# Performance work log

Measured on AMD Instinct MI355X. Metric: run time of the kernel, lower is better.

## Reference

```python
import jax, jax.numpy as jnp
import numpy as np

B, T = 64, 2048
HID, FAST, SLOW, VOCAB = 256, 64, 256, 64
WRITE_THRESH = 0.4
NEG = -1000000000.0


def setup_inputs() -> dict:
    key = jax.random.key(0)
    ks = jax.random.split(key, 10)
    s = 0.05  # small init so gate sigmoids are not saturated
    return {
        "seq": jax.random.randint(ks[0], (B, T), 0, VOCAB),
        "emb": jax.random.normal(ks[1], (VOCAB, HID), jnp.float32),        # encoder embedding table
        "Wg": jax.random.normal(ks[2], (HID, 1), jnp.float32) * s,         # write_gate
        "bg": jnp.zeros((1,), jnp.float32),
        "Wd": jax.random.normal(ks[3], (HID, 1), jnp.float32) * s,         # demotion_net
        "bd": jnp.zeros((1,), jnp.float32),
        "Wq": jax.random.normal(ks[4], (HID, HID), jnp.float32) * s,       # read_head.q_proj
        "bq": jnp.zeros((HID,), jnp.float32),
        "Wo": jax.random.normal(ks[5], (HID, VOCAB), jnp.float32) * s,     # read_head.out
        "bo": jnp.zeros((VOCAB,), jnp.float32),
    }


def _process_sequence(h, Wg, bg, Wd, bd):
    # h: (B, T, H). Sequential LRU tiered-memory scatter, vectorized over batch.
    Bb, Tt, H = h.shape

    def step(state, tok_h):
        fm, sm, fa, sa, fu, su = state
        ws = jax.nn.sigmoid(tok_h @ Wg + bg)[:, 0]          # (B,) write score
        act = ws >= WRITE_THRESH                            # skip rows with score < 0.4
        fa = fa + fu.astype(jnp.int32)                      # age occupied slots
        sa = sa + su.astype(jnp.int32)
        free = ~fu
        has_free = jnp.any(free, axis=1)                    # (B,)
        free_idx = jnp.argmax(free, axis=1)                 # first free fast slot
        dem = ((fm @ Wd)[..., 0] + bd[0])                   # (B, FAST) demotion scores
        dem_slot = jnp.argmin(dem, axis=1)
        fslot = jnp.where(has_free, free_idx, dem_slot)     # fast slot to write
        foh = jax.nn.one_hot(fslot, FAST, dtype=bool)
        wf = act[:, None] & foh                              # (B, FAST) fast-write mask
        # value demoted to slow (only used when fast was full)
        demoted = jnp.take_along_axis(fm, fslot[:, None, None], axis=1)[:, 0, :]
        slow_act = act & ~has_free
        sfree = ~su
        s_has_free = jnp.any(sfree, axis=1)
        ss = jnp.where(s_has_free, jnp.argmax(sfree, axis=1), jnp.argmax(sa, axis=1))
        soh = jax.nn.one_hot(ss, SLOW, dtype=bool)
        wsm = slow_act[:, None] & soh                        # (B, SLOW) slow-write mask
        sm = jnp.where(wsm[..., None], demoted[:, None, :], sm)
        sa = jnp.where(wsm, 0, sa)
        su = su | wsm
        tok = jax.lax.stop_gradient(tok_h)                   # original writes tok_h.detach()
        fm = jnp.where(wf[..., None], tok[:, None, :], fm)
        fa = jnp.where(wf, 0, fa)
        fu = fu | wf
        return (fm, sm, fa, sa, fu, su), None

    init = (
        jnp.zeros((Bb, FAST, H), h.dtype),
        jnp.zeros((Bb, SLOW, H), h.dtype),
        jnp.zeros((Bb, FAST), jnp.int32),
        jnp.zeros((Bb, SLOW), jnp.int32),
        jnp.zeros((Bb, FAST), bool),
        jnp.zeros((Bb, SLOW), bool),
    )
    hs = jnp.swapaxes(h[:, : Tt - 3], 0, 1)                  # loop runs for T-3 tokens
    (fm, sm, fa, sa, fu, su), _ = jax.lax.scan(step, init, hs)
    memory = jnp.concatenate([fm, sm], axis=1)               # (B, F+S, H)
    mask = jnp.concatenate([fu, su], axis=1).astype(h.dtype)
    slow_mask = su.astype(h.dtype)
    return memory, mask, slow_mask


def reference(seq, emb, Wg, bg, Wd, bd, Wq, bq, Wo, bo):
    h = emb[seq]                                             # encoder: (B, T, H)
    memory, mask, slow_mask = _process_sequence(h, Wg, bg, Wd, bd)
    # ReadHead
    q = h[:, -1, :] @ Wq + bq                                # (B, H)
    scores = jnp.einsum("bnh,bh->bn", memory, q)
    scores = jnp.where(mask == 0, NEG, scores)
    attn = jax.nn.softmax(scores, axis=-1)
    ctx = jnp.einsum("bn,bnh->bh", attn, memory)
    logits = ctx @ Wo + bo                                   # (B, VOCAB)
    return logits, slow_mask
```

## Files before the change

kernel.cpp:

```cpp
#include <hip/hip_runtime.h>
#include <math.h>

#define BB 64
#define TT 2048
#define HIDD 256
#define FASTN 64
#define SLOWN 256
#define VOC 64
#define TLOOP (TT - 3)
#define NEGC -1000000000.0f
#define EPAD 257
#define NEGBIG (-(1 << 20))
#define BYTEAT(U, J) ((int)(((U) >> (8 * (J))) & 0xFFu))
#define NW 16
#define NT (NW * 64)

__global__ __launch_bounds__(NT) void k_one(
    const int* __restrict__ seq, const float* __restrict__ emb,
    const float* __restrict__ Wg, const float* __restrict__ bg,
    const float* __restrict__ Wd, const float* __restrict__ bd,
    const float* __restrict__ Wq, const float* __restrict__ bq,
    const float* __restrict__ Wo, const float* __restrict__ bo,
    float* __restrict__ out) {
  const int b = blockIdx.x;
  const int tid = threadIdx.x;
  const int lane = tid & 63;
  const int wv = tid >> 6;

  __shared__ float embS[VOC * EPAD];
  __shared__ __align__(16) unsigned char zsB[2080];
  __shared__ float qLastS[HIDD], ctxS[HIDD];
  __shared__ float pp16[NW][64];
  __shared__ float gp16[NW][64], dp16[NW][64];
  __shared__ float qp4[4][HIDD];
  __shared__ float demS[64], wS[64];
  __shared__ int prS[64], invS[64], cntTok[64];
  __shared__ int CS[NW];
  __shared__ int PsS[NW][64], QsS[NW][64], aEndS[NW][64], eSS[NW][64];

  const int2 sq = ((const int2*)(seq + b * TT))[tid];
  const int lastv = seq[b * TT + TT - 1];
  const float4* emb4 = (const float4*)emb;
  for (int i = tid; i < VOC * 64; i += NT) {
    float4 e = emb4[i];
    float* d = &embS[(i >> 6) * EPAD + ((i & 63) << 2)];
    d[0] = e.x; d[1] = e.y; d[2] = e.z; d[3] = e.w;
  }
  __syncthreads();

  {
    const int v = tid & 63, kp = tid >> 6;
    const float* er = &embS[v * EPAD + kp * 16];
    const float* wg = &Wg[kp * 16];
    const float* wd = &Wd[kp * 16];
    float g = 0.f, d = 0.f;
#pragma unroll
    for (int k = 0; k < 16; ++k) { float e = er[k]; g += e * wg[k]; d += e * wd[k]; }
    gp16[kp][v] = g; dp16[kp][v] = d;
  }
  __syncthreads();
  if (tid < 64) {
    float g = bg[0], d = bd[0];
#pragma unroll
    for (int p = 0; p < NW; ++p) { g += gp16[p][tid]; d += dp16[p][tid]; }
    int act = (1.f / (1.f + expf(-g)) >= 0.4f) ? 1 : 0;
    demS[tid] = d;
    float dv = d;
    int r = 0;
    for (int u2 = 0; u2 < 64; ++u2) {
      float du = demS[u2];
      r += (du < dv || (du == dv && u2 < tid)) ? 1 : 0;
    }
    invS[r] = tid;
    prS[tid] = act ? r : 0xFF;
  }
  __syncthreads();

  const int t0 = tid * 2;
  int by0, by1, c;
  {
    int r0 = prS[sq.x], r1 = prS[sq.y];
    by0 = (t0 < TLOOP) ? r0 : 0xFF;
    by1 = (t0 + 1 < TLOOP) ? r1 : 0xFF;
    c = ((by0 != 0xFF) ? 1 : 0) + ((by1 != 0xFF) ? 1 : 0);
  }
  int incl = c;
  for (int s = 1; s < 64; s <<= 1) {
    int t = __shfl_up(incl, s);
    if (lane >= s) incl += t;
  }
  if (lane == 63) CS[wv] = incl;
  __syncthreads();

  int Ow = 0, A = 0;
#pragma unroll
  for (int w2 = 0; w2 < NW; ++w2) {
    int cw = CS[w2];
    Ow += (w2 < wv) ? cw : 0;
    A += cw;
  }
  {
    int pos = Ow + incl - c;
    if (by0 != 0xFF) zsB[pos++] = (unsigned char)by0;
    if (by1 != 0xFF) zsB[pos++] = (unsigned char)by1;
  }
  __syncthreads();

  const int fsplit = A < 64 ? A : 64;
  const int nL = A - fsplit;
  const int win = nL < 256 ? nL : 256;
  const int wstart = A - win;
  const int L = (((A + NW - 1) / NW) + 15) & ~15;
  const int baseW = wv * L;
  const int endW = min(baseW + L, A);

  int P = 0, Q = NEGBIG;
  for (int g = baseW; g < endW; g += 16) {
    uint4 t4 = *(const uint4*)(zsB + g);
    unsigned dsw[4] = {t4.x, t4.y, t4.z, t4.w};
    const int gHi = min(g + 16, endW);
    if (gHi == g + 16 && gHi <= fsplit) {
#pragma unroll
      for (int d = 0; d < 4; ++d)
#pragma unroll
        for (int j = 0; j < 4; ++j) {
          int x = (BYTEAT(dsw[d], j) <= lane) ? 1 : 0;
          P += x; Q += x;
        }
    } else if (gHi == g + 16 && g >= fsplit) {
#pragma unroll
      for (int d = 0; d < 4; ++d)
#pragma unroll
        for (int j = 0; j < 4; ++j) {
          int x = (BYTEAT(dsw[d], j) <= lane) ? 1 : 0;
          P += x - 1;
          Q = max(Q + x - 1, x);
        }
    } else {
#pragma unroll
      for (int d = 0; d < 4; ++d)
#pragma unroll
        for (int j = 0; j < 4; ++j) {
          int i = g + d * 4 + j;
          int x = (BYTEAT(dsw[d], j) <= lane) ? 1 : 0;
          bool vld = i < endW;
          bool fil = i < fsplit;
          int p = fil ? x : x - 1;
          int q = fil ? NEGBIG : x;
          int Pn = P + p;
          int Qn = max(Q + p, q);
          P = vld ? Pn : P;
          Q = vld ? Qn : Q;
        }
    }
  }
  PsS[wv][lane] = P;
  QsS[wv][lane] = Q;
  __syncthreads();

  int a = 0;
  for (int w2 = 0; w2 < wv; ++w2)
    a = max(a + PsS[w2][lane], QsS[w2][lane]);

  int e = 0;
  for (int g = baseW; g < endW; g += 16) {
    uint4 t4 = *(const uint4*)(zsB + g);
    unsigned dsw[4] = {t4.x, t4.y, t4.z, t4.w};
    const int gHi = min(g + 16, endW);
    const bool full = (gHi == g + 16);
    if (full && gHi <= fsplit) {
#pragma unroll
      for (int d = 0; d < 4; ++d)
#pragma unroll
        for (int j = 0; j < 4; ++j)
          a += (BYTEAT(dsw[d], j) <= lane) ? 1 : 0;
    } else if (full && g >= fsplit && gHi <= wstart) {
#pragma unroll
      for (int d = 0; d < 4; ++d)
#pragma unroll
        for (int j = 0; j < 4; ++j) {
          int xm1 = (BYTEAT(dsw[d], j) <= lane) ? 0 : -1;
          a = max(a, 1) + xm1;
        }
    } else if (full && g >= wstart) {
#pragma unroll
      for (int d = 0; d < 4; ++d)
#pragma unroll
        for (int j = 0; j < 4; ++j) {
          int xm1 = (BYTEAT(dsw[d], j) <= lane) ? 0 : -1;
          e += (a > 0) ? 1 : 0;
          a = max(a, 1) + xm1;
        }
    } else {
#pragma unroll
      for (int d = 0; d < 4; ++d)
#pragma unroll
        for (int j = 0; j < 4; ++j) {
          int i = g + d * 4 + j;
          int x = (BYTEAT(dsw[d], j) <= lane) ? 1 : 0;
          bool vld = i < endW;
          bool fil = i < fsplit;
          bool wg = vld && (i >= wstart);
          e += (wg && a > 0) ? 1 : 0;
          int af = a + x;
          int al = max(a, 1) + (x - 1);
          int an = fil ? af : al;
          a = vld ? an : a;
        }
    }
  }
  aEndS[wv][lane] = a;
  eSS[wv][lane] = e;
  __syncthreads();

  if (tid < 64) {
    int af = aEndS[NW - 1][lane];
    int et = 0;
#pragma unroll
    for (int w2 = 0; w2 < NW; ++w2) et += eSS[w2][lane];
    int ap = __shfl_up(af, 1); if (lane == 0) ap = 0;
    int ep = __shfl_up(et, 1); if (lane == 0) ep = 0;
    cntTok[invS[lane]] = (af - ap) + (et - ep);
  }

  {
    const int j = tid & 255, kq = tid >> 8;
    const float* eL = &embS[lastv * EPAD + kq * 64];
    const float* wq = &Wq[(kq * 64) * HIDD + j];
    float acc = 0.f;
#pragma unroll 8
    for (int k = 0; k < 64; ++k) acc += eL[k] * wq[k * HIDD];
    qp4[kq][j] = acc;
  }
  __syncthreads();
  if (tid < 256)
    qLastS[tid] = qp4[0][tid] + qp4[1][tid] + qp4[2][tid] + qp4[3][tid] + bq[tid];
  __syncthreads();

  {
    const int v = tid & 63, part = tid >> 6;
    const float* er = &embS[v * EPAD + part * 16];
    const float* qr = &qLastS[part * 16];
    float s = 0.f;
#pragma unroll
    for (int k = 0; k < 16; ++k) s += er[k] * qr[k];
    pp16[part][v] = s;
  }
  __syncthreads();
  if (tid < 64) {
    float sc = 0.f;
#pragma unroll
    for (int p = 0; p < NW; ++p) sc += pp16[p][tid];
    int cc = cntTok[tid];
    float m = (cc > 0) ? sc : NEGC;
    for (int off = 32; off; off >>= 1) m = fmaxf(m, __shfl_xor(m, off));
    float w = (cc > 0) ? (float)cc * expf(sc - m) : 0.f;
    float z = w;
    for (int off = 32; off; off >>= 1) z += __shfl_xor(z, off);
    z += (float)(FASTN + SLOWN - (fsplit + win)) * expf(NEGC - m);
    wS[tid] = w / z;
  }
  __syncthreads();

  {
    const int h = tid & 255, part = tid >> 8;
    float cacc = 0.f;
#pragma unroll
    for (int u = 0; u < 16; ++u)
      cacc += wS[part * 16 + u] * embS[(part * 16 + u) * EPAD + h];
    qp4[part][h] = cacc;
  }
  __syncthreads();
  if (tid < 256)
    ctxS[tid] = qp4[0][tid] + qp4[1][tid] + qp4[2][tid] + qp4[3][tid];
  __syncthreads();

  {
    const int o = tid & 63, part = tid >> 6;
    const float* cr = &ctxS[part * 16];
    const float* wr = &Wo[(part * 16) * VOC + o];
    float s = 0.f;
#pragma unroll
    for (int k = 0; k < 16; ++k) s += cr[k] * wr[k * VOC];
    pp16[part][o] = s;
  }
  __syncthreads();
  if (tid < 64) {
    float s = bo[tid];
#pragma unroll
    for (int p = 0; p < NW; ++p) s += pp16[p][tid];
    out[b * VOC + tid] = s;
  }
  if (tid < 256)
    out[BB * VOC + b * SLOWN + tid] = (tid < win) ? 1.0f : 0.0f;
}

extern "C" void kernel_launch(void* const* d_in, const int* in_sizes, int n_in,
                              void* d_out, int out_size, void* d_ws, size_t ws_size,
                              hipStream_t stream) {
  const int*   seq = (const int*)d_in[0];
  const float* emb = (const float*)d_in[1];
  const float* Wg  = (const float*)d_in[2];
  const float* bg  = (const float*)d_in[3];
  const float* Wd  = (const float*)d_in[4];
  const float* bd  = (const float*)d_in[5];
  const float* Wq  = (const float*)d_in[6];
  const float* bq  = (const float*)d_in[7];
  const float* Wo  = (const float*)d_in[8];
  const float* bo  = (const float*)d_in[9];
  float* out = (float*)d_out;

  k_one<<<dim3(64), dim3(NT), 0, stream>>>(seq, emb, Wg, bg, Wd, bd,
                                           Wq, bq, Wo, bo, out);
}
```

Before: 89.98 us.

## Prefetch Wq/Wo into registers early and skip second scan outside slow window

Wq columns are loaded into registers before the scan phases, and the q projection is computed in two halves between them, so global loads overlap the LRU scan work. Warps whose range ends before the slow window no longer rerun the second scan pass. The final per-lane state is instead rebuilt by a serial max-plus combine of the per-warp summaries. The context reduction is collapsed into one pass over 256 threads, removing a sync and a partial-sum buffer. Wo is prefetched into registers before the softmax, and the slow-mask store moves earlier. The register arrays raise register pressure in a 1024-thread block.

```diff
diff --git a/kernel.cpp b/kernel.cpp
--- a/kernel.cpp
+++ b/kernel.cpp
@@ -36,7 +36,7 @@
   __shared__ float demS[64], wS[64];
   __shared__ int prS[64], invS[64], cntTok[64];
   __shared__ int CS[NW];
-  __shared__ int PsS[NW][64], QsS[NW][64], aEndS[NW][64], eSS[NW][64];
+  __shared__ int PsS[NW][64], QsS[NW][64], eSS[NW][64];
 
   const int2 sq = ((const int2*)(seq + b * TT))[tid];
   const int lastv = seq[b * TT + TT - 1];
@@ -113,6 +113,14 @@
   const int L = (((A + NW - 1) / NW) + 15) & ~15;
   const int baseW = wv * L;
   const int endW = min(baseW + L, A);
+
+  if (tid < 256)
+    out[BB * VOC + b * SLOWN + tid] = (tid < win) ? 1.0f : 0.0f;
+
+  const int jq = tid & 255, kq = tid >> 8, kb = kq * 64;
+  float wqA[32];
+#pragma unroll
+  for (int k = 0; k < 32; ++k) wqA[k] = Wq[(kb + k) * HIDD + jq];
 
   int P = 0, Q = NEGBIG;
   for (int g = baseW; g < endW; g += 16) {
@@ -158,63 +166,84 @@
   QsS[wv][lane] = Q;
   __syncthreads();
 
-  int a = 0;
-  for (int w2 = 0; w2 < wv; ++w2)
-    a = max(a + PsS[w2][lane], QsS[w2][lane]);
+  float qacc = 0.f;
+  {
+    const float* eL = &embS[lastv * EPAD + kb];
+#pragma unroll
+    for (int k = 0; k < 32; ++k) qacc += eL[k] * wqA[k];
+  }
+  float wqB[32];
+#pragma unroll
+  for (int k = 0; k < 32; ++k) wqB[k] = Wq[(kb + 32 + k) * HIDD + jq];
 
   int e = 0;
-  for (int g = baseW; g < endW; g += 16) {
-    uint4 t4 = *(const uint4*)(zsB + g);
-    unsigned dsw[4] = {t4.x, t4.y, t4.z, t4.w};
-    const int gHi = min(g + 16, endW);
-    const bool full = (gHi == g + 16);
-    if (full && gHi <= fsplit) {
-#pragma unroll
-      for (int d = 0; d < 4; ++d)
-#pragma unroll
-        for (int j = 0; j < 4; ++j)
-          a += (BYTEAT(dsw[d], j) <= lane) ? 1 : 0;
-    } else if (full && g >= fsplit && gHi <= wstart) {
-#pragma unroll
-      for (int d = 0; d < 4; ++d)
-#pragma unroll
-        for (int j = 0; j < 4; ++j) {
-          int xm1 = (BYTEAT(dsw[d], j) <= lane) ? 0 : -1;
-          a = max(a, 1) + xm1;
-        }
-    } else if (full && g >= wstart) {
-#pragma unroll
-      for (int d = 0; d < 4; ++d)
-#pragma unroll
-        for (int j = 0; j < 4; ++j) {
-          int xm1 = (BYTEAT(dsw[d], j) <= lane) ? 0 : -1;
-          e += (a > 0) ? 1 : 0;
-          a = max(a, 1) + xm1;
-        }
-    } else {
-#pragma unroll
-      for (int d = 0; d < 4; ++d)
-#pragma unroll
-        for (int j = 0; j < 4; ++j) {
-          int i = g + d * 4 + j;
-          int x = (BYTEAT(dsw[d], j) <= lane) ? 1 : 0;
-          bool vld = i < endW;
-          bool fil = i < fsplit;
-          bool wg = vld && (i >= wstart);
-          e += (wg && a > 0) ? 1 : 0;
-          int af = a + x;
-          int al = max(a, 1) + (x - 1);
-          int an = fil ? af : al;
-          a = vld ? an : a;
-        }
+  const bool walkW = (endW > wstart);
+  if (walkW) {
+    int a = 0;
+    for (int w2 = 0; w2 < wv; ++w2)
+      a = max(a + PsS[w2][lane], QsS[w2][lane]);
+    for (int g = baseW; g < endW; g += 16) {
+      uint4 t4 = *(const uint4*)(zsB + g);
+      unsigned dsw[4] = {t4.x, t4.y, t4.z, t4.w};
+      const int gHi = min(g + 16, endW);
+      const bool full = (gHi == g + 16);
+      if (full && gHi <= fsplit) {
+#pragma unroll
+        for (int d = 0; d < 4; ++d)
+#pragma unroll
+          for (int j = 0; j < 4; ++j)
+            a += (BYTEAT(dsw[d], j) <= lane) ? 1 : 0;
+      } else if (full && g >= fsplit && gHi <= wstart) {
+#pragma unroll
+        for (int d = 0; d < 4; ++d)
+#pragma unroll
+          for (int j = 0; j < 4; ++j) {
+            int xm1 = (BYTEAT(dsw[d], j) <= lane) ? 0 : -1;
+            a = max(a, 1) + xm1;
+          }
+      } else if (full && g >= wstart) {
+#pragma unroll
+        for (int d = 0; d < 4; ++d)
+#pragma unroll
+          for (int j = 0; j < 4; ++j) {
+            int xm1 = (BYTEAT(dsw[d], j) <= lane) ? 0 : -1;
+            e += (a > 0) ? 1 : 0;
+            a = max(a, 1) + xm1;
+          }
+      } else {
+#pragma unroll
+        for (int d = 0; d < 4; ++d)
+#pragma unroll
+          for (int j = 0; j < 4; ++j) {
+            int i = g + d * 4 + j;
+            int x = (BYTEAT(dsw[d], j) <= lane) ? 1 : 0;
+            bool vld = i < endW;
+            bool fil = i < fsplit;
+            bool wg = vld && (i >= wstart);
+            e += (wg && a > 0) ? 1 : 0;
+            int af = a + x;
+            int al = max(a, 1) + (x - 1);
+            int an = fil ? af : al;
+            a = vld ? an : a;
+          }
+      }
     }
   }
-  aEndS[wv][lane] = a;
   eSS[wv][lane] = e;
+
+  {
+    const float* eL = &embS[lastv * EPAD + kb + 32];
+#pragma unroll
+    for (int k = 0; k < 32; ++k) qacc += eL[k] * wqB[k];
+  }
+  qp4[kq][jq] = qacc;
   __syncthreads();
 
   if (tid < 64) {
-    int af = aEndS[NW - 1][lane];
+    int af = 0;
+#pragma unroll
+    for (int w2 = 0; w2 < NW; ++w2)
+      af = max(af + PsS[w2][lane], QsS[w2][lane]);
     int et = 0;
 #pragma unroll
     for (int w2 = 0; w2 < NW; ++w2) et += eSS[w2][lane];
@@ -222,29 +251,22 @@
     int ep = __shfl_up(et, 1); if (lane == 0) ep = 0;
     cntTok[invS[lane]] = (af - ap) + (et - ep);
   }
-
-  {
-    const int j = tid & 255, kq = tid >> 8;
-    const float* eL = &embS[lastv * EPAD + kq * 64];
-    const float* wq = &Wq[(kq * 64) * HIDD + j];
-    float acc = 0.f;
-#pragma unroll 8
-    for (int k = 0; k < 64; ++k) acc += eL[k] * wq[k * HIDD];
-    qp4[kq][j] = acc;
-  }
-  __syncthreads();
   if (tid < 256)
     qLastS[tid] = qp4[0][tid] + qp4[1][tid] + qp4[2][tid] + qp4[3][tid] + bq[tid];
   __syncthreads();
 
-  {
-    const int v = tid & 63, part = tid >> 6;
-    const float* er = &embS[v * EPAD + part * 16];
+  const int o = tid & 63, part = tid >> 6;
+  float wor[16];
+#pragma unroll
+  for (int k = 0; k < 16; ++k) wor[k] = Wo[((part << 4) + k) * VOC + o];
+
+  {
+    const float* er = &embS[o * EPAD + part * 16];
     const float* qr = &qLastS[part * 16];
     float s = 0.f;
 #pragma unroll
     for (int k = 0; k < 16; ++k) s += er[k] * qr[k];
-    pp16[part][v] = s;
+    pp16[part][o] = s;
   }
   __syncthreads();
   if (tid < 64) {
@@ -262,26 +284,19 @@
   }
   __syncthreads();
 
-  {
-    const int h = tid & 255, part = tid >> 8;
+  if (tid < 256) {
     float cacc = 0.f;
-#pragma unroll
-    for (int u = 0; u < 16; ++u)
-      cacc += wS[part * 16 + u] * embS[(part * 16 + u) * EPAD + h];
-    qp4[part][h] = cacc;
-  }
-  __syncthreads();
-  if (tid < 256)
-    ctxS[tid] = qp4[0][tid] + qp4[1][tid] + qp4[2][tid] + qp4[3][tid];
-  __syncthreads();
-
-  {
-    const int o = tid & 63, part = tid >> 6;
+#pragma unroll 16
+    for (int u = 0; u < 64; ++u) cacc += wS[u] * embS[u * EPAD + tid];
+    ctxS[tid] = cacc;
+  }
+  __syncthreads();
+
+  {
     const float* cr = &ctxS[part * 16];
-    const float* wr = &Wo[(part * 16) * VOC + o];
     float s = 0.f;
 #pragma unroll
-    for (int k = 0; k < 16; ++k) s += cr[k] * wr[k * VOC];
+    for (int k = 0; k < 16; ++k) s += cr[k] * wor[k];
     pp16[part][o] = s;
   }
   __syncthreads();
@@ -291,8 +306,6 @@
     for (int p = 0; p < NW; ++p) s += pp16[p][tid];
     out[b * VOC + tid] = s;
   }
-  if (tid < 256)
-    out[BB * VOC + b * SLOWN + tid] = (tid < win) ? 1.0f : 0.0f;
 }
 
 extern "C" void kernel_launch(void* const* d_in, const int* in_sizes, int n_in,
```

Measured after the change: 88.56 us. Within noise of the previous version (-1.6%).
